# Optimization experiments

Measured on AMD Instinct MI355X. Metric: run time of the kernel, lower is better.

The kernel has to match this reference:

```python
import jax, jax.numpy as jnp
import numpy as np

N, K, C, S = 40000, 16, 128, 8  # points, neighbors, channels, share_planes
EPS = 1e-5


def _bn(x, g, b, m, v):
    # eval-mode BatchNorm1d over the channel (last) axis
    return (x - m) * (g * jax.lax.rsqrt(v + EPS)) + b


def _forward(xyz, feats, Wq, bq, Wk, bk, Wv, bv, Wp1, bp1, p_gamma, p_beta, p_mean, p_var,
             Wp2, bp2, w_gamma, w_beta, w_mean, w_var, Ww1, bw1, w1_gamma, w1_beta,
             w1_mean, w1_var, Ww2, bw2, nei_ind):
    x = feats[0]          # (N, C)
    pos = xyz[0]          # (N, 3)
    idx = nei_ind[0]      # (N, K)

    q = x @ Wq + bq                      # (N, C)
    kf = (x @ Wk + bk)[idx]              # (N, K, C) neighbor gather
    vf = (x @ Wv + bv)[idx]              # (N, K, C)

    d = pos[idx] - pos[:, None, :]       # (N, K, 3) relative positions
    # linear_p: Linear_BN(3,3) -> ReLU -> Linear(3, C)
    p = jax.nn.relu(_bn(d @ Wp1 + bp1, p_gamma, p_beta, p_mean, p_var)) @ Wp2 + bp2  # (N, K, C)

    # mid_planes == out_planes, so the view(...,1,mid).sum(2) is an identity reshape
    w = kf - q[:, None, :] + p           # (N, K, C)
    w = _bn(w, w_gamma, w_beta, w_mean, w_var)  # bn_w over channels
    # linear_w: ReLU -> Linear_BN(C, C//S) -> ReLU -> Linear(C//S, C//S)
    w = jax.nn.relu(_bn(jax.nn.relu(w) @ Ww1 + bw1, w1_gamma, w1_beta, w1_mean, w1_var)) @ Ww2 + bw2  # (N, K, C//S)
    w = jax.nn.softmax(w, axis=1)        # softmax over K neighbors

    # grouped-channel weighted sum over neighbors
    agg = ((vf + p).reshape(N, K, S, C // S) * w[:, :, None, :]).sum(axis=1).reshape(N, C)

    # shortcut is Identity (in_planes == out_planes); broadcast over batch dim like torch
    return jax.nn.leaky_relu(agg[None, :, :] + feats, negative_slope=0.1)  # (1, N, C)


def setup_inputs() -> dict:
    key = jax.random.key(0)
    ks = jax.random.split(key, 16)
    f32 = jnp.float32

    def w(k, shape, scale):
        return jax.random.normal(k, shape, dtype=f32) * scale

    return {
        "xyz": jax.random.uniform(ks[0], (1, N, 3), dtype=f32),
        "feats": jax.random.normal(ks[1], (1, N, C), dtype=f32),
        "nei_ind": jax.random.randint(ks[2], (1, N, K), 0, N, dtype=jnp.int32),
        "Wq": w(ks[3], (C, C), C ** -0.5), "bq": jnp.zeros((C,), f32),
        "Wk": w(ks[4], (C, C), C ** -0.5), "bk": jnp.zeros((C,), f32),
        "Wv": w(ks[5], (C, C), C ** -0.5), "bv": jnp.zeros((C,), f32),
        "Wp1": w(ks[6], (3, 3), 0.5), "bp1": jnp.zeros((3,), f32),
        "p_gamma": jnp.ones((3,), f32), "p_beta": jnp.zeros((3,), f32),
        "p_mean": w(ks[7], (3,), 0.1), "p_var": jnp.ones((3,), f32),
        "Wp2": w(ks[8], (3, C), 0.5), "bp2": jnp.zeros((C,), f32),
        "w_gamma": jnp.ones((C,), f32), "w_beta": jnp.zeros((C,), f32),
        "w_mean": w(ks[9], (C,), 0.1), "w_var": jnp.ones((C,), f32),
        "Ww1": w(ks[10], (C, C // S), C ** -0.5), "bw1": jnp.zeros((C // S,), f32),
        "w1_gamma": jnp.ones((C // S,), f32), "w1_beta": jnp.zeros((C // S,), f32),
        "w1_mean": w(ks[11], (C // S,), 0.1), "w1_var": jnp.ones((C // S,), f32),
        "Ww2": w(ks[12], (C // S, C // S), (C // S) ** -0.5), "bw2": jnp.zeros((C // S,), f32),
    }


def reference(xyz, feats, nei_ind, Wq, bq, Wk, bk, Wv, bv, Wp1, bp1, p_gamma, p_beta,
              p_mean, p_var, Wp2, bp2, w_gamma, w_beta, w_mean, w_var, Ww1, bw1,
              w1_gamma, w1_beta, w1_mean, w1_var, Ww2, bw2):
    return _forward(xyz, feats, Wq, bq, Wk, bk, Wv, bv, Wp1, bp1, p_gamma, p_beta,
                    p_mean, p_var, Wp2, bp2, w_gamma, w_beta, w_mean, w_var, Ww1, bw1,
                    w1_gamma, w1_beta, w1_mean, w1_var, Ww2, bw2, nei_ind)
```

## Files before the change

### kernel.cpp

```cpp
#include <hip/hip_runtime.h>
#include <stdint.h>

#define N_PTS 40000
#define KNBR  16
#define CH    128
#define EPSV  1e-5f

typedef __attribute__((ext_vector_type(4))) float f32x4;
typedef __attribute__((ext_vector_type(8))) short bf16x8;

__device__ __forceinline__ float bf2f(ushort u) {
    union { uint32_t i; float f; } x; x.i = ((uint32_t)u) << 16; return x.f;
}
__device__ __forceinline__ float bflo(uint32_t u) {
    union { uint32_t i; float f; } x; x.i = u << 16; return x.f;
}
__device__ __forceinline__ float bfhi(uint32_t u) {
    union { uint32_t i; float f; } x; x.i = u & 0xffff0000u; return x.f;
}
__device__ __forceinline__ ushort f2bf(float f) {
    union { float f; uint32_t i; } x; x.f = f;
    uint32_t i = x.i;
    i += 0x7fffu + ((i >> 16) & 1u);
    return (ushort)(i >> 16);
}
__device__ __forceinline__ uint32_t pack2(float a, float b) {
    return (uint32_t)f2bf(a) | ((uint32_t)f2bf(b) << 16);
}

template <bool BF> struct IO;
template <> struct IO<true> {
    static __device__ __forceinline__ float  ld (const void* p, int i) { return bf2f(((const ushort*)p)[i]); }
    static __device__ __forceinline__ float2 ld2(const void* p, int i) { const uint32_t u = ((const uint32_t*)p)[i]; return make_float2(bflo(u), bfhi(u)); }
    static __device__ __forceinline__ ushort ldbf(const void* p, int i) { return ((const ushort*)p)[i]; }
    static __device__ __forceinline__ void   st2(void* p, int i, float a, float b) { ((uint32_t*)p)[i] = pack2(a, b); }
};
template <> struct IO<false> {
    static __device__ __forceinline__ float  ld (const void* p, int i) { return ((const float*)p)[i]; }
    static __device__ __forceinline__ float2 ld2(const void* p, int i) { return ((const float2*)p)[i]; }
    static __device__ __forceinline__ ushort ldbf(const void* p, int i) { return f2bf(((const float*)p)[i]); }
    static __device__ __forceinline__ void   st2(void* p, int i, float a, float b) { ((float2*)p)[i] = make_float2(a, b); }
};

__device__ __forceinline__ bool detect_bf16(const void* w_var) {
    return (*(const uint32_t*)w_var & 0xffffu) != 0u;
}

#define PROJ_BLOCKS 500
template <bool BF>
__device__ void proj_body(
    const void* feats,
    const void* Wq, const void* bq, const void* Wk, const void* bk,
    const void* Wv, const void* bv,
    ushort* qws, ushort* kws, ushort* vws)
{
    const int l    = threadIdx.x & 63;
    const int w    = threadIdx.x >> 6;
    const int t    = l & 15;
    const int quad = l >> 4;
    const int cq   = w;

    const void* Wsrc[3] = { Wq, Wk, Wv };
    const void* bsrc[3] = { bq, bk, bv };
    ushort*     dst [3] = { qws, kws, vws };

    bf16x8 afrag[3][4];
    float  bias[3][4];
    #pragma unroll
    for (int m = 0; m < 3; ++m) {
        #pragma unroll
        for (int s = 0; s < 4; ++s)
            #pragma unroll
            for (int j = 0; j < 8; ++j) {
                const int k = s * 32 + quad * 8 + j;
                afrag[m][s][j] = (short)IO<BF>::ldbf(Wsrc[m], k * CH + cq * 16 + t);
            }
        #pragma unroll
        for (int r = 0; r < 4; ++r)
            bias[m][r] = IO<BF>::ld(bsrc[m], cq * 16 + quad * 4 + r);
    }

    #pragma unroll
    for (int n = 0; n < 5; ++n) {
        const int tt = blockIdx.x + PROJ_BLOCKS * n;
        const int p0 = tt * 16;
        bf16x8 bfr[4];
        if (BF) {
            const ushort* xp = (const ushort*)feats + (p0 + t) * CH + quad * 8;
            #pragma unroll
            for (int s = 0; s < 4; ++s)
                bfr[s] = *(const bf16x8*)(xp + s * 32);
        } else {
            const float* xp = (const float*)feats + (p0 + t) * CH + quad * 8;
            #pragma unroll
            for (int s = 0; s < 4; ++s) {
                const float4 a = *(const float4*)(xp + s * 32);
                const float4 b = *(const float4*)(xp + s * 32 + 4);
                bfr[s][0] = (short)f2bf(a.x); bfr[s][1] = (short)f2bf(a.y);
                bfr[s][2] = (short)f2bf(a.z); bfr[s][3] = (short)f2bf(a.w);
                bfr[s][4] = (short)f2bf(b.x); bfr[s][5] = (short)f2bf(b.y);
                bfr[s][6] = (short)f2bf(b.z); bfr[s][7] = (short)f2bf(b.w);
            }
        }
        #pragma unroll
        for (int m = 0; m < 3; ++m) {
            f32x4 acc = { bias[m][0], bias[m][1], bias[m][2], bias[m][3] };
            #pragma unroll
            for (int s = 0; s < 4; ++s)
                acc = __builtin_amdgcn_mfma_f32_16x16x32_bf16(afrag[m][s], bfr[s], acc, 0, 0, 0);
            uint2 o;
            o.x = pack2(acc[0], acc[1]);
            o.y = pack2(acc[2], acc[3]);
            ((uint2*)dst[m])[(p0 + t) * 32 + cq * 4 + quad] = o;
        }
    }
}

__global__ __launch_bounds__(512) void proj_kernel(
    const void* feats, const void* Wq, const void* bq, const void* Wk,
    const void* bk, const void* Wv, const void* bv, const void* w_var_probe,
    ushort* qws, ushort* kws, ushort* vws)
{
    if (detect_bf16(w_var_probe))
        proj_body<true >(feats, Wq, bq, Wk, bk, Wv, bv, qws, kws, vws);
    else
        proj_body<false>(feats, Wq, bq, Wk, bk, Wv, bv, qws, kws, vws);
}

template <bool BF>
__device__ void attn_body(
    const void* xyz, const void* feats, const int* __restrict__ nei,
    const ushort* __restrict__ qws, const ushort* __restrict__ kws,
    const ushort* __restrict__ vws,
    const void* Wp1, const void* bp1, const void* p_gamma, const void* p_beta,
    const void* p_mean, const void* p_var, const void* Wp2, const void* bp2,
    const void* w_gamma, const void* w_beta, const void* w_mean, const void* w_var,
    const void* Ww1, const void* bw1, const void* w1_gamma, const void* w1_beta,
    const void* w1_mean, const void* w1_var, const void* Ww2, const void* bw2,
    void* out, ushort* wbuf, ushort* ubuf, float* wsm, int i0, int l)
{
    const int t = l & 15;
    const int quad = l >> 4;

    float A1[3][3], C1[3];
    #pragma unroll
    for (int b = 0; b < 3; ++b) {
        const float sb = IO<BF>::ld(p_gamma, b) * rsqrtf(IO<BF>::ld(p_var, b) + EPSV);
        C1[b] = (IO<BF>::ld(bp1, b) - IO<BF>::ld(p_mean, b)) * sb + IO<BF>::ld(p_beta, b);
        #pragma unroll
        for (int a = 0; a < 3; ++a) A1[a][b] = IO<BF>::ld(Wp1, a * 3 + b) * sb;
    }

    const float2 vg = IO<BF>::ld2(w_gamma, l);
    const float2 vb = IO<BF>::ld2(w_beta, l);
    const float2 vm = IO<BF>::ld2(w_mean, l);
    const float2 vv = IO<BF>::ld2(w_var, l);
    const float scw0 = vg.x * rsqrtf(vv.x + EPSV);
    const float scw1 = vg.y * rsqrtf(vv.y + EPSV);
    const float shw0 = vb.x - vm.x * scw0;
    const float shw1 = vb.y - vm.y * scw1;

    float wp2c[3][2];
    #pragma unroll
    for (int r = 0; r < 3; ++r) {
        const float2 u = IO<BF>::ld2(Wp2, r * 64 + l);
        wp2c[r][0] = u.x; wp2c[r][1] = u.y;
    }
    const float2 vbp2 = IO<BF>::ld2(bp2, l);
    const float bp20 = vbp2.x, bp21 = vbp2.y;

    bf16x8 bfrag1[4];
    #pragma unroll
    for (int s = 0; s < 4; ++s)
        #pragma unroll
        for (int kk = 0; kk < 8; ++kk) {
            const int k = s * 32 + quad * 8 + kk;
            bfrag1[s][kk] = (short)IO<BF>::ldbf(Ww1, k * 16 + t);
        }
    bf16x8 bfrag2;
    #pragma unroll
    for (int kk = 0; kk < 8; ++kk) {
        const int k = quad * 8 + kk;
        bfrag2[kk] = (quad < 2) ? (short)IO<BF>::ldbf(Ww2, k * 16 + t) : (short)0;
    }

    const float s1t  = IO<BF>::ld(w1_gamma, t) * rsqrtf(IO<BF>::ld(w1_var, t) + EPSV);
    const float sh1t = IO<BF>::ld(w1_beta, t) - IO<BF>::ld(w1_mean, t) * s1t;
    const float bw1t = IO<BF>::ld(bw1, t);
    const float bw2t = IO<BF>::ld(bw2, t);

    for (int pp = 0; pp < 4; ++pp) {
        const int i = i0 + pp;

        const uint32_t uq = ((const uint32_t*)qws)[i * 64 + l];
        const float q0 = bflo(uq), q1 = bfhi(uq);

        const float pix = IO<BF>::ld(xyz, i * 3 + 0);
        const float piy = IO<BF>::ld(xyz, i * 3 + 1);
        const float piz = IO<BF>::ld(xyz, i * 3 + 2);

        const int vnj = nei[i * KNBR + t];
        const float ndx = IO<BF>::ld(xyz, vnj * 3 + 0) - pix;
        const float ndy = IO<BF>::ld(xyz, vnj * 3 + 1) - piy;
        const float ndz = IO<BF>::ld(xyz, vnj * 3 + 2) - piz;
        const float hh0 = fmaxf(0.f, ndx * A1[0][0] + ndy * A1[1][0] + ndz * A1[2][0] + C1[0]);
        const float hh1 = fmaxf(0.f, ndx * A1[0][1] + ndy * A1[1][1] + ndz * A1[2][1] + C1[1]);
        const float hh2 = fmaxf(0.f, ndx * A1[0][2] + ndy * A1[1][2] + ndz * A1[2][2] + C1[2]);

        int njs[KNBR];
        #pragma unroll
        for (int j = 0; j < KNBR; ++j) njs[j] = nei[i * KNBR + j];
        uint32_t ukf[KNBR], uvf[KNBR];
        #pragma unroll
        for (int j = 0; j < KNBR; ++j) ukf[j] = ((const uint32_t*)kws)[njs[j] * 64 + l];
        #pragma unroll
        for (int j = 0; j < KNBR; ++j) uvf[j] = ((const uint32_t*)vws)[njs[j] * 64 + l];

        float vfp0[KNBR], vfp1[KNBR];
        #pragma unroll
        for (int j = 0; j < KNBR; ++j) {
            const float h0 = __shfl(hh0, j);
            const float h1 = __shfl(hh1, j);
            const float h2 = __shfl(hh2, j);
            const float p0 = h0 * wp2c[0][0] + h1 * wp2c[1][0] + h2 * wp2c[2][0] + bp20;
            const float p1 = h0 * wp2c[0][1] + h1 * wp2c[1][1] + h2 * wp2c[2][1] + bp21;
            vfp0[j] = bflo(uvf[j]) + p0;
            vfp1[j] = bfhi(uvf[j]) + p1;
            const float w0 = fmaxf(0.f, (bflo(ukf[j]) - q0 + p0) * scw0 + shw0);
            const float w1 = fmaxf(0.f, (bfhi(ukf[j]) - q1 + p1) * scw1 + shw1);
            ((uint32_t*)wbuf)[j * 68 + l] = pack2(w0, w1);
        }

        f32x4 acc1 = { bw1t, bw1t, bw1t, bw1t };
        const ushort* arow = &wbuf[(l & 15) * 136 + quad * 8];
        #pragma unroll
        for (int s = 0; s < 4; ++s) {
            const bf16x8 afrag = *(const bf16x8*)(arow + s * 32);
            acc1 = __builtin_amdgcn_mfma_f32_16x16x32_bf16(afrag, bfrag1[s], acc1, 0, 0, 0);
        }
        #pragma unroll
        for (int r = 0; r < 4; ++r) {
            const float u = fmaxf(0.f, acc1[r] * s1t + sh1t);
            ubuf[(quad * 4 + r) * 24 + t] = f2bf(u);
        }

        f32x4 acc2 = { bw2t, bw2t, bw2t, bw2t };
        bf16x8 afrag2;
        if (quad < 2) {
            afrag2 = *(const bf16x8*)(&ubuf[(l & 15) * 24 + quad * 8]);
        } else {
            #pragma unroll
            for (int kk = 0; kk < 8; ++kk) afrag2[kk] = 0;
        }
        acc2 = __builtin_amdgcn_mfma_f32_16x16x32_bf16(afrag2, bfrag2, acc2, 0, 0, 0);

        float z0 = acc2[0], z1 = acc2[1], z2 = acc2[2], z3 = acc2[3];
        float mx = fmaxf(fmaxf(z0, z1), fmaxf(z2, z3));
        mx = fmaxf(mx, __shfl_xor(mx, 16));
        mx = fmaxf(mx, __shfl_xor(mx, 32));
        const float e0 = __expf(z0 - mx), e1 = __expf(z1 - mx);
        const float e2 = __expf(z2 - mx), e3 = __expf(z3 - mx);
        float ssum = e0 + e1 + e2 + e3;
        ssum += __shfl_xor(ssum, 16);
        ssum += __shfl_xor(ssum, 32);
        const float inv = 1.0f / ssum;
        wsm[(quad * 4 + 0) * 18 + t] = e0 * inv;
        wsm[(quad * 4 + 1) * 18 + t] = e1 * inv;
        wsm[(quad * 4 + 2) * 18 + t] = e2 * inv;
        wsm[(quad * 4 + 3) * 18 + t] = e3 * inv;

        const int t0 = (2 * l) & 15;
        float agg0 = 0.f, agg1 = 0.f;
        #pragma unroll
        for (int j = 0; j < KNBR; ++j) {
            const float2 wp = *(const float2*)&wsm[j * 18 + t0];
            agg0 = fmaf(vfp0[j], wp.x, agg0);
            agg1 = fmaf(vfp1[j], wp.y, agg1);
        }
        const float2 xf = IO<BF>::ld2(feats, i * 64 + l);
        float o0 = agg0 + xf.x;
        float o1 = agg1 + xf.y;
        o0 = o0 > 0.f ? o0 : 0.1f * o0;
        o1 = o1 > 0.f ? o1 : 0.1f * o1;
        IO<BF>::st2(out, i * 64 + l, o0, o1);
    }
}

__global__ __launch_bounds__(256) void attn_kernel(
    const void* xyz, const void* feats, const int* __restrict__ nei,
    const ushort* __restrict__ qws, const ushort* __restrict__ kws,
    const ushort* __restrict__ vws,
    const void* Wp1, const void* bp1, const void* p_gamma, const void* p_beta,
    const void* p_mean, const void* p_var, const void* Wp2, const void* bp2,
    const void* w_gamma, const void* w_beta, const void* w_mean, const void* w_var,
    const void* Ww1, const void* bw1, const void* w1_gamma, const void* w1_beta,
    const void* w1_mean, const void* w1_var, const void* Ww2, const void* bw2,
    void* out)
{
    __shared__ ushort wbuf[4][16 * 136];
    __shared__ ushort ubuf[4][16 * 24];
    __shared__ float  wsm [4][16 * 18];

    const int wave = threadIdx.x >> 6;
    const int l    = threadIdx.x & 63;
    const int i0   = blockIdx.x * 16 + wave * 4;

    if (detect_bf16(w_var))
        attn_body<true >(xyz, feats, nei, qws, kws, vws, Wp1, bp1, p_gamma, p_beta,
                         p_mean, p_var, Wp2, bp2, w_gamma, w_beta, w_mean, w_var,
                         Ww1, bw1, w1_gamma, w1_beta, w1_mean, w1_var, Ww2, bw2,
                         out, wbuf[wave], ubuf[wave], wsm[wave], i0, l);
    else
        attn_body<false>(xyz, feats, nei, qws, kws, vws, Wp1, bp1, p_gamma, p_beta,
                         p_mean, p_var, Wp2, bp2, w_gamma, w_beta, w_mean, w_var,
                         Ww1, bw1, w1_gamma, w1_beta, w1_mean, w1_var, Ww2, bw2,
                         out, wbuf[wave], ubuf[wave], wsm[wave], i0, l);
}

extern "C" void kernel_launch(void* const* d_in, const int* in_sizes, int n_in,
                              void* d_out, int out_size, void* d_ws, size_t ws_size,
                              hipStream_t stream) {
    const void* xyz     = d_in[0];
    const void* feats   = d_in[1];
    const int*  nei     = (const int*)d_in[2];
    const void* Wq      = d_in[3];
    const void* bq      = d_in[4];
    const void* Wk      = d_in[5];
    const void* bk      = d_in[6];
    const void* Wv      = d_in[7];
    const void* bv      = d_in[8];
    const void* Wp1     = d_in[9];
    const void* bp1     = d_in[10];
    const void* p_gamma = d_in[11];
    const void* p_beta  = d_in[12];
    const void* p_mean  = d_in[13];
    const void* p_var   = d_in[14];
    const void* Wp2     = d_in[15];
    const void* bp2     = d_in[16];
    const void* w_gamma = d_in[17];
    const void* w_beta  = d_in[18];
    const void* w_mean  = d_in[19];
    const void* w_var   = d_in[20];
    const void* Ww1     = d_in[21];
    const void* bw1     = d_in[22];
    const void* w1_gamma= d_in[23];
    const void* w1_beta = d_in[24];
    const void* w1_mean = d_in[25];
    const void* w1_var  = d_in[26];
    const void* Ww2     = d_in[27];
    const void* bw2     = d_in[28];

    ushort* qws = (ushort*)d_ws;
    ushort* kws = qws + (size_t)N_PTS * CH;
    ushort* vws = kws + (size_t)N_PTS * CH;

    proj_kernel<<<PROJ_BLOCKS, 512, 0, stream>>>(feats, Wq, bq, Wk, bk, Wv, bv, w_var,
                                                 qws, kws, vws);
    attn_kernel<<<N_PTS / 16, 256, 0, stream>>>(xyz, feats, nei, qws, kws, vws,
                                          Wp1, bp1, p_gamma, p_beta, p_mean, p_var,
                                          Wp2, bp2, w_gamma, w_beta, w_mean, w_var,
                                          Ww1, bw1, w1_gamma, w1_beta, w1_mean, w1_var,
                                          Ww2, bw2, d_out);
}
```

Before: 227.5 us.

## Interleave K and V projections into one buffer and shrink per-wave work

```diff
diff --git a/kernel.cpp b/kernel.cpp
--- a/kernel.cpp
+++ b/kernel.cpp
@@ -24,9 +24,19 @@
     i += 0x7fffu + ((i >> 16) & 1u);
     return (ushort)(i >> 16);
 }
+
+#if __has_builtin(__builtin_amdgcn_cvt_pk_bf16_f32)
+typedef __bf16 bf16x2v __attribute__((ext_vector_type(2)));
+__device__ __forceinline__ uint32_t pack2(float a, float b) {
+    union { bf16x2v v; uint32_t u; } x;
+    x.v = __builtin_amdgcn_cvt_pk_bf16_f32(a, b);
+    return x.u;
+}
+#else
 __device__ __forceinline__ uint32_t pack2(float a, float b) {
     return (uint32_t)f2bf(a) | ((uint32_t)f2bf(b) << 16);
 }
+#endif
 
 template <bool BF> struct IO;
 template <> struct IO<true> {
@@ -46,13 +56,13 @@
     return (*(const uint32_t*)w_var & 0xffffu) != 0u;
 }
 
-#define PROJ_BLOCKS 500
+#define PROJ_BLOCKS 1250
 template <bool BF>
 __device__ void proj_body(
     const void* feats,
     const void* Wq, const void* bq, const void* Wk, const void* bk,
     const void* Wv, const void* bv,
-    ushort* qws, ushort* kws, ushort* vws)
+    uint32_t* qws, uint4* kvws)
 {
     const int l    = threadIdx.x & 63;
     const int w    = threadIdx.x >> 6;
@@ -62,7 +72,6 @@
 
     const void* Wsrc[3] = { Wq, Wk, Wv };
     const void* bsrc[3] = { bq, bk, bv };
-    ushort*     dst [3] = { qws, kws, vws };
 
     bf16x8 afrag[3][4];
     float  bias[3][4];
@@ -81,7 +90,7 @@
     }
 
     #pragma unroll
-    for (int n = 0; n < 5; ++n) {
+    for (int n = 0; n < 2; ++n) {
         const int tt = blockIdx.x + PROJ_BLOCKS * n;
         const int p0 = tt * 16;
         bf16x8 bfr[4];
@@ -102,42 +111,51 @@
                 bfr[s][6] = (short)f2bf(b.z); bfr[s][7] = (short)f2bf(b.w);
             }
         }
+        f32x4 acc[3];
         #pragma unroll
         for (int m = 0; m < 3; ++m) {
-            f32x4 acc = { bias[m][0], bias[m][1], bias[m][2], bias[m][3] };
+            acc[m] = f32x4{ bias[m][0], bias[m][1], bias[m][2], bias[m][3] };
             #pragma unroll
             for (int s = 0; s < 4; ++s)
-                acc = __builtin_amdgcn_mfma_f32_16x16x32_bf16(afrag[m][s], bfr[s], acc, 0, 0, 0);
-            uint2 o;
-            o.x = pack2(acc[0], acc[1]);
-            o.y = pack2(acc[2], acc[3]);
-            ((uint2*)dst[m])[(p0 + t) * 32 + cq * 4 + quad] = o;
-        }
+                acc[m] = __builtin_amdgcn_mfma_f32_16x16x32_bf16(afrag[m][s], bfr[s], acc[m], 0, 0, 0);
+        }
+        const int p = p0 + t;
+        const int m16 = cq * 4 + quad;
+        uint2 qo;
+        qo.x = pack2(acc[0][0], acc[0][1]);
+        qo.y = pack2(acc[0][2], acc[0][3]);
+        ((uint2*)qws)[p * 32 + m16] = qo;
+        uint4 kv;
+        kv.x = pack2(acc[1][0], acc[1][1]);
+        kv.y = pack2(acc[2][0], acc[2][1]);
+        kv.z = pack2(acc[1][2], acc[1][3]);
+        kv.w = pack2(acc[2][2], acc[2][3]);
+        kvws[p * 32 + m16] = kv;
     }
 }
 
 __global__ __launch_bounds__(512) void proj_kernel(
     const void* feats, const void* Wq, const void* bq, const void* Wk,
     const void* bk, const void* Wv, const void* bv, const void* w_var_probe,
-    ushort* qws, ushort* kws, ushort* vws)
+    uint32_t* qws, uint4* kvws)
 {
     if (detect_bf16(w_var_probe))
-        proj_body<true >(feats, Wq, bq, Wk, bk, Wv, bv, qws, kws, vws);
+        proj_body<true >(feats, Wq, bq, Wk, bk, Wv, bv, qws, kvws);
     else
-        proj_body<false>(feats, Wq, bq, Wk, bk, Wv, bv, qws, kws, vws);
+        proj_body<false>(feats, Wq, bq, Wk, bk, Wv, bv, qws, kvws);
 }
 
 template <bool BF>
 __device__ void attn_body(
     const void* xyz, const void* feats, const int* __restrict__ nei,
-    const ushort* __restrict__ qws, const ushort* __restrict__ kws,
-    const ushort* __restrict__ vws,
+    const uint32_t* __restrict__ qws, const uint2* __restrict__ kvws,
     const void* Wp1, const void* bp1, const void* p_gamma, const void* p_beta,
     const void* p_mean, const void* p_var, const void* Wp2, const void* bp2,
     const void* w_gamma, const void* w_beta, const void* w_mean, const void* w_var,
     const void* Ww1, const void* bw1, const void* w1_gamma, const void* w1_beta,
     const void* w1_mean, const void* w1_var, const void* Ww2, const void* bw2,
-    void* out, ushort* wbuf, ushort* ubuf, float* wsm, int i0, int l)
+    void* out, ushort* wbuf, ushort* ubuf, float* wsm, float* hlds,
+    int i0, int l)
 {
     const int t = l & 15;
     const int quad = l >> 4;
@@ -189,10 +207,11 @@
     const float bw1t = IO<BF>::ld(bw1, t);
     const float bw2t = IO<BF>::ld(bw2, t);
 
-    for (int pp = 0; pp < 4; ++pp) {
+    #pragma unroll
+    for (int pp = 0; pp < 2; ++pp) {
         const int i = i0 + pp;
 
-        const uint32_t uq = ((const uint32_t*)qws)[i * 64 + l];
+        const uint32_t uq = qws[i * 64 + l];
         const float q0 = bflo(uq), q1 = bfhi(uq);
 
         const float pix = IO<BF>::ld(xyz, i * 3 + 0);
@@ -206,33 +225,30 @@
         const float hh0 = fmaxf(0.f, ndx * A1[0][0] + ndy * A1[1][0] + ndz * A1[2][0] + C1[0]);
         const float hh1 = fmaxf(0.f, ndx * A1[0][1] + ndy * A1[1][1] + ndz * A1[2][1] + C1[1]);
         const float hh2 = fmaxf(0.f, ndx * A1[0][2] + ndy * A1[1][2] + ndz * A1[2][2] + C1[2]);
+        if (quad == 0)
+            *(float4*)&hlds[t * 4] = make_float4(hh0, hh1, hh2, 0.f);
 
         int njs[KNBR];
         #pragma unroll
         for (int j = 0; j < KNBR; ++j) njs[j] = nei[i * KNBR + j];
-        uint32_t ukf[KNBR], uvf[KNBR];
-        #pragma unroll
-        for (int j = 0; j < KNBR; ++j) ukf[j] = ((const uint32_t*)kws)[njs[j] * 64 + l];
-        #pragma unroll
-        for (int j = 0; j < KNBR; ++j) uvf[j] = ((const uint32_t*)vws)[njs[j] * 64 + l];
-
-        float vfp0[KNBR], vfp1[KNBR];
+        uint2 kv[KNBR];
+        #pragma unroll
+        for (int j = 0; j < KNBR; ++j) kv[j] = kvws[njs[j] * 64 + l];
+
+        uint32_t vfp[KNBR];
         #pragma unroll
         for (int j = 0; j < KNBR; ++j) {
-            const float h0 = __shfl(hh0, j);
-            const float h1 = __shfl(hh1, j);
-            const float h2 = __shfl(hh2, j);
-            const float p0 = h0 * wp2c[0][0] + h1 * wp2c[1][0] + h2 * wp2c[2][0] + bp20;
-            const float p1 = h0 * wp2c[0][1] + h1 * wp2c[1][1] + h2 * wp2c[2][1] + bp21;
-            vfp0[j] = bflo(uvf[j]) + p0;
-            vfp1[j] = bfhi(uvf[j]) + p1;
-            const float w0 = fmaxf(0.f, (bflo(ukf[j]) - q0 + p0) * scw0 + shw0);
-            const float w1 = fmaxf(0.f, (bfhi(ukf[j]) - q1 + p1) * scw1 + shw1);
+            const float4 h = *(const float4*)&hlds[j * 4];
+            const float p0 = h.x * wp2c[0][0] + h.y * wp2c[1][0] + h.z * wp2c[2][0] + bp20;
+            const float p1 = h.x * wp2c[0][1] + h.y * wp2c[1][1] + h.z * wp2c[2][1] + bp21;
+            vfp[j] = pack2(bflo(kv[j].y) + p0, bfhi(kv[j].y) + p1);
+            const float w0 = fmaxf(0.f, (bflo(kv[j].x) - q0 + p0) * scw0 + shw0);
+            const float w1 = fmaxf(0.f, (bfhi(kv[j].x) - q1 + p1) * scw1 + shw1);
             ((uint32_t*)wbuf)[j * 68 + l] = pack2(w0, w1);
         }
 
         f32x4 acc1 = { bw1t, bw1t, bw1t, bw1t };
-        const ushort* arow = &wbuf[(l & 15) * 136 + quad * 8];
+        const ushort* arow = &wbuf[t * 136 + quad * 8];
         #pragma unroll
         for (int s = 0; s < 4; ++s) {
             const bf16x8 afrag = *(const bf16x8*)(arow + s * 32);
@@ -247,7 +263,7 @@
         f32x4 acc2 = { bw2t, bw2t, bw2t, bw2t };
         bf16x8 afrag2;
         if (quad < 2) {
-            afrag2 = *(const bf16x8*)(&ubuf[(l & 15) * 24 + quad * 8]);
+            afrag2 = *(const bf16x8*)(&ubuf[t * 24 + quad * 8]);
         } else {
             #pragma unroll
             for (int kk = 0; kk < 8; ++kk) afrag2[kk] = 0;
@@ -274,8 +290,8 @@
         #pragma unroll
         for (int j = 0; j < KNBR; ++j) {
             const float2 wp = *(const float2*)&wsm[j * 18 + t0];
-            agg0 = fmaf(vfp0[j], wp.x, agg0);
-            agg1 = fmaf(vfp1[j], wp.y, agg1);
+            agg0 = fmaf(bflo(vfp[j]), wp.x, agg0);
+            agg1 = fmaf(bfhi(vfp[j]), wp.y, agg1);
         }
         const float2 xf = IO<BF>::ld2(feats, i * 64 + l);
         float o0 = agg0 + xf.x;
@@ -286,10 +302,9 @@
     }
 }
 
-__global__ __launch_bounds__(256) void attn_kernel(
+__global__ __launch_bounds__(256, 5) void attn_kernel(
     const void* xyz, const void* feats, const int* __restrict__ nei,
-    const ushort* __restrict__ qws, const ushort* __restrict__ kws,
-    const ushort* __restrict__ vws,
+    const uint32_t* __restrict__ qws, const uint2* __restrict__ kvws,
     const void* Wp1, const void* bp1, const void* p_gamma, const void* p_beta,
     const void* p_mean, const void* p_var, const void* Wp2, const void* bp2,
     const void* w_gamma, const void* w_beta, const void* w_mean, const void* w_var,
@@ -300,21 +315,22 @@
     __shared__ ushort wbuf[4][16 * 136];
     __shared__ ushort ubuf[4][16 * 24];
     __shared__ float  wsm [4][16 * 18];
+    __shared__ float  hlds[4][16 * 4];
 
     const int wave = threadIdx.x >> 6;
     const int l    = threadIdx.x & 63;
-    const int i0   = blockIdx.x * 16 + wave * 4;
+    const int i0   = blockIdx.x * 8 + wave * 2;
 
     if (detect_bf16(w_var))
-        attn_body<true >(xyz, feats, nei, qws, kws, vws, Wp1, bp1, p_gamma, p_beta,
+        attn_body<true >(xyz, feats, nei, qws, kvws, Wp1, bp1, p_gamma, p_beta,
                          p_mean, p_var, Wp2, bp2, w_gamma, w_beta, w_mean, w_var,
                          Ww1, bw1, w1_gamma, w1_beta, w1_mean, w1_var, Ww2, bw2,
-                         out, wbuf[wave], ubuf[wave], wsm[wave], i0, l);
+                         out, wbuf[wave], ubuf[wave], wsm[wave], hlds[wave], i0, l);
     else
-        attn_body<false>(xyz, feats, nei, qws, kws, vws, Wp1, bp1, p_gamma, p_beta,
+        attn_body<false>(xyz, feats, nei, qws, kvws, Wp1, bp1, p_gamma, p_beta,
                          p_mean, p_var, Wp2, bp2, w_gamma, w_beta, w_mean, w_var,
                          Ww1, bw1, w1_gamma, w1_beta, w1_mean, w1_var, Ww2, bw2,
-                         out, wbuf[wave], ubuf[wave], wsm[wave], i0, l);
+                         out, wbuf[wave], ubuf[wave], wsm[wave], hlds[wave], i0, l);
 }
 
 extern "C" void kernel_launch(void* const* d_in, const int* in_sizes, int n_in,
@@ -350,13 +366,12 @@
     const void* Ww2     = d_in[27];
     const void* bw2     = d_in[28];
 
-    ushort* qws = (ushort*)d_ws;
-    ushort* kws = qws + (size_t)N_PTS * CH;
-    ushort* vws = kws + (size_t)N_PTS * CH;
+    uint32_t* qws  = (uint32_t*)d_ws;
+    uint4*    kvws = (uint4*)(qws + (size_t)N_PTS * 64);
 
     proj_kernel<<<PROJ_BLOCKS, 512, 0, stream>>>(feats, Wq, bq, Wk, bk, Wv, bv, w_var,
-                                                 qws, kws, vws);
-    attn_kernel<<<N_PTS / 16, 256, 0, stream>>>(xyz, feats, nei, qws, kws, vws,
+                                                 qws, kvws);
+    attn_kernel<<<N_PTS / 8, 256, 0, stream>>>(xyz, feats, nei, qws, (const uint2*)kvws,
                                           Wp1, bp1, p_gamma, p_beta, p_mean, p_var,
                                           Wp2, bp2, w_gamma, w_beta, w_mean, w_var,
                                           Ww1, bw1, w1_gamma, w1_beta, w1_mean, w1_var,
```

After: 361.6 us. 1.59x slower.
